# Optimization experiments

Hardware: AMD Instinct MI355X
Metric: run time of the kernel (lower is better)

Reference implementation:

```python
import jax, jax.numpy as jnp
import numpy as np

S, P, C = 64, 2048, 32   # num_scenes, num_pixels, scene_channels
A, D, E = 2048, 128, 64  # agent_size, dynamics_features, embed_dim


def setup_inputs() -> dict:
    key = jax.random.key(0)
    ks = jax.random.split(key, 9)
    inv = lambda n: 1.0 / np.sqrt(n)
    return {
        "global_scene": jax.random.normal(ks[0], (S, P, C), jnp.float32),
        "scene_idx": jax.random.randint(ks[1], (A,), 0, S),
        "dynamic_encoding": jax.random.normal(ks[2], (A, D), jnp.float32),
        "W_sn": jax.random.uniform(ks[3], (C, E), jnp.float32, -inv(C), inv(C)),
        "b_sn": jax.random.uniform(ks[4], (E,), jnp.float32, -inv(C), inv(C)),
        "W_df": jax.random.uniform(ks[5], (D, E), jnp.float32, -inv(D), inv(D)),
        "b_df": jax.random.uniform(ks[6], (E,), jnp.float32, -inv(D), inv(D)),
        "w_fc": jax.random.uniform(ks[7], (E,), jnp.float32, -inv(E), inv(E)),
        "b_fc": jax.random.uniform(ks[8], (1,), jnp.float32, -inv(E), inv(E)),
    }


def reference(global_scene, scene_idx, dynamic_encoding, W_sn, b_sn, W_df, b_df, w_fc, b_fc):
    # att1: [S, P, E]; att2: [A, E]
    att1 = jnp.einsum('spc,ce->spe', global_scene, W_sn) + b_sn
    att2 = dynamic_encoding @ W_df + b_df
    # gather scenes per agent, fuse add + relu: [A, P, E]
    add_fusion = jax.nn.relu(att1[scene_idx] + att2[:, None, :])
    # linear to scalar score per pixel, softmax over pixels (dim=1)
    logits = jnp.einsum('ape,e->ap', add_fusion, w_fc) + b_fc[0]  # [A, P]
    alpha = jax.nn.softmax(logits, axis=1)[:, :, None]            # [A, P, 1]
    # alpha-weighted pooling of gathered scene features -> [A, C]
    return jnp.sum(alpha * global_scene[scene_idx], axis=1)
```

## Files before the change

### kernel.cpp

```cpp
#include <hip/hip_runtime.h>
#include <hip/hip_bf16.h>

#define S_ 64
#define P_ 2048
#define C_ 32
#define A_ 2048
#define D_ 128
#define E_ 64

#define LPX   64
#define NLCH  (P_ / LPX)

__global__ __launch_bounds__(256) void att2s_kernel(
    const float* __restrict__ de, const float* __restrict__ Wdf,
    const float* __restrict__ bdf, const int* __restrict__ sidx,
    float* __restrict__ att2, int* __restrict__ counts,
    int* __restrict__ lists) {
  __shared__ float4 Wl[128 * 16];
  __shared__ float4 bl[16];
  __shared__ float  dl[16 * 128];
  const int tid = threadIdx.x;

  if (tid < 16) {
    const int a = blockIdx.x * 16 + tid;
    const int s = sidx[a];
    const int pos = atomicAdd(&counts[s], 1);
    lists[s * A_ + pos] = a;
  }

  const float4* W4 = (const float4*)Wdf;
#pragma unroll
  for (int i = 0; i < 8; ++i) Wl[tid + i * 256] = W4[tid + i * 256];
  if (tid < 16) bl[tid] = ((const float4*)bdf)[tid];
  const long base = (long)blockIdx.x * (16 * 128);
#pragma unroll
  for (int i = 0; i < 8; ++i) dl[tid + i * 256] = de[base + tid + i * 256];
  __syncthreads();

  const int r = tid >> 4, e4 = tid & 15;
  float4 acc = bl[e4];
#pragma unroll 4
  for (int d = 0; d < 128; ++d) {
    const float  g = dl[r * 128 + d];
    const float4 w = Wl[d * 16 + e4];
    acc.x = fmaf(g, w.x, acc.x);
    acc.y = fmaf(g, w.y, acc.y);
    acc.z = fmaf(g, w.z, acc.z);
    acc.w = fmaf(g, w.w, acc.w);
  }
  ((float4*)att2)[((long)blockIdx.x * 16 + r) * 16 + e4] = acc;
}

__global__ __launch_bounds__(256) void fused_kernel(
    const float* __restrict__ gs, const float* __restrict__ Wsn,
    const float* __restrict__ bsn, const float* __restrict__ wfc,
    const float* __restrict__ att2, const int* __restrict__ counts,
    const int* __restrict__ lists, float* __restrict__ out,
    float* __restrict__ Z) {
  const int s   = blockIdx.x >> 5;
  const int p0  = (blockIdx.x & (NLCH - 1)) * LPX;
  const int tid = threadIdx.x;
  const int px  = tid >> 2;
  const int eq  = tid & 3;

  __shared__ float  gsl[LPX][36];
  __shared__ float4 Wl4[32 * 16];
  __shared__ float4 a2l[32][16];
  __shared__ float  alpha_l[32][64];
  __shared__ int    aidl[32];

  const float4* W4 = (const float4*)Wsn;
  Wl4[tid]       = W4[tid];
  Wl4[tid + 256] = W4[tid + 256];

  const float4* g4 = (const float4*)(gs + ((long)s * P_ + p0) * C_);
#pragma unroll
  for (int k = 0; k < 2; ++k) {
    const int f = tid + k * 256;
    const float4 v = g4[f];
    const int pp = f >> 3, c0 = (f & 7) * 4;
    gsl[pp][c0]     = v.x;
    gsl[pp][c0 + 1] = v.y;
    gsl[pp][c0 + 2] = v.z;
    gsl[pp][c0 + 3] = v.w;
  }

  const float4* wf4 = (const float4*)wfc;
  const float4* b4  = (const float4*)bsn;
  float4 wf[4], a1[4];
#pragma unroll
  for (int q = 0; q < 4; ++q) { wf[q] = wf4[eq * 4 + q]; a1[q] = b4[eq * 4 + q]; }
  __syncthreads();

#pragma unroll
  for (int c = 0; c < 32; ++c) {
    const float g = gsl[px][c];
#pragma unroll
    for (int q = 0; q < 4; ++q) {
      const float4 w = Wl4[c * 16 + eq * 4 + q];
      a1[q].x = fmaf(g, w.x, a1[q].x);
      a1[q].y = fmaf(g, w.y, a1[q].y);
      a1[q].z = fmaf(g, w.z, a1[q].z);
      a1[q].w = fmaf(g, w.w, a1[q].w);
    }
  }

  const int j2 = tid >> 3;
  const int c4 = tid & 7;
  const int n_s = counts[s];

  for (int g0 = 0; g0 < n_s; g0 += 32) {
    const int m = min(32, n_s - g0);
    __syncthreads();
    if (tid < m) aidl[tid] = lists[s * A_ + g0 + tid];
    __syncthreads();
#pragma unroll
    for (int k = 0; k < 2; ++k) {
      const int idx = tid + k * 256;
      const int j = idx >> 4, e4 = idx & 15;
      if (j < m) a2l[j][e4] = ((const float4*)att2)[aidl[j] * 16 + e4];
    }
    __syncthreads();

    for (int j = 0; j < m; ++j) {
      const float4 t0 = a2l[j][eq * 4 + 0];
      const float4 t1 = a2l[j][eq * 4 + 1];
      const float4 t2 = a2l[j][eq * 4 + 2];
      const float4 t3 = a2l[j][eq * 4 + 3];
      float c0 = 0.f, c1 = 0.f, c2 = 0.f, c3 = 0.f;
      c0 = fmaf(fmaxf(a1[0].x + t0.x, 0.f), wf[0].x, c0);
      c1 = fmaf(fmaxf(a1[0].y + t0.y, 0.f), wf[0].y, c1);
      c2 = fmaf(fmaxf(a1[0].z + t0.z, 0.f), wf[0].z, c2);
      c3 = fmaf(fmaxf(a1[0].w + t0.w, 0.f), wf[0].w, c3);
      c0 = fmaf(fmaxf(a1[1].x + t1.x, 0.f), wf[1].x, c0);
      c1 = fmaf(fmaxf(a1[1].y + t1.y, 0.f), wf[1].y, c1);
      c2 = fmaf(fmaxf(a1[1].z + t1.z, 0.f), wf[1].z, c2);
      c3 = fmaf(fmaxf(a1[1].w + t1.w, 0.f), wf[1].w, c3);
      c0 = fmaf(fmaxf(a1[2].x + t2.x, 0.f), wf[2].x, c0);
      c1 = fmaf(fmaxf(a1[2].y + t2.y, 0.f), wf[2].y, c1);
      c2 = fmaf(fmaxf(a1[2].z + t2.z, 0.f), wf[2].z, c2);
      c3 = fmaf(fmaxf(a1[2].w + t2.w, 0.f), wf[2].w, c3);
      c0 = fmaf(fmaxf(a1[3].x + t3.x, 0.f), wf[3].x, c0);
      c1 = fmaf(fmaxf(a1[3].y + t3.y, 0.f), wf[3].y, c1);
      c2 = fmaf(fmaxf(a1[3].z + t3.z, 0.f), wf[3].z, c2);
      c3 = fmaf(fmaxf(a1[3].w + t3.w, 0.f), wf[3].w, c3);
      float r = (c0 + c1) + (c2 + c3);
      r += __shfl_xor(r, 1);
      r += __shfl_xor(r, 2);
      if (eq == 0) alpha_l[j][px] = __expf(r);
    }
    __syncthreads();

    if (j2 < m) {
      const int a = aidl[j2];
      float4 a0 = make_float4(0.f, 0.f, 0.f, 0.f);
      float4 a1p = make_float4(0.f, 0.f, 0.f, 0.f);
      float4 a2p = make_float4(0.f, 0.f, 0.f, 0.f);
      float4 a3p = make_float4(0.f, 0.f, 0.f, 0.f);
      float  zs = 0.f;
#pragma unroll 4
      for (int p4 = 0; p4 < LPX / 4; ++p4) {
        const float w0 = alpha_l[j2][p4 * 4 + 0];
        const float w1 = alpha_l[j2][p4 * 4 + 1];
        const float w2 = alpha_l[j2][p4 * 4 + 2];
        const float w3 = alpha_l[j2][p4 * 4 + 3];
        const float4 v0 = *(const float4*)&gsl[p4 * 4 + 0][c4 * 4];
        const float4 v1 = *(const float4*)&gsl[p4 * 4 + 1][c4 * 4];
        const float4 v2 = *(const float4*)&gsl[p4 * 4 + 2][c4 * 4];
        const float4 v3 = *(const float4*)&gsl[p4 * 4 + 3][c4 * 4];
        zs += (w0 + w1) + (w2 + w3);
        a0.x = fmaf(w0, v0.x, a0.x); a0.y = fmaf(w0, v0.y, a0.y);
        a0.z = fmaf(w0, v0.z, a0.z); a0.w = fmaf(w0, v0.w, a0.w);
        a1p.x = fmaf(w1, v1.x, a1p.x); a1p.y = fmaf(w1, v1.y, a1p.y);
        a1p.z = fmaf(w1, v1.z, a1p.z); a1p.w = fmaf(w1, v1.w, a1p.w);
        a2p.x = fmaf(w2, v2.x, a2p.x); a2p.y = fmaf(w2, v2.y, a2p.y);
        a2p.z = fmaf(w2, v2.z, a2p.z); a2p.w = fmaf(w2, v2.w, a2p.w);
        a3p.x = fmaf(w3, v3.x, a3p.x); a3p.y = fmaf(w3, v3.y, a3p.y);
        a3p.z = fmaf(w3, v3.z, a3p.z); a3p.w = fmaf(w3, v3.w, a3p.w);
      }
      const float4 acc = make_float4((a0.x + a1p.x) + (a2p.x + a3p.x),
                                     (a0.y + a1p.y) + (a2p.y + a3p.y),
                                     (a0.z + a1p.z) + (a2p.z + a3p.z),
                                     (a0.w + a1p.w) + (a2p.w + a3p.w));
      float* op = out + (long)a * C_ + c4 * 4;
      atomicAdd(op,     acc.x);
      atomicAdd(op + 1, acc.y);
      atomicAdd(op + 2, acc.z);
      atomicAdd(op + 3, acc.w);
      if (c4 == 0) atomicAdd(&Z[a], zs);
    }
  }
}

__global__ __launch_bounds__(256) void norm_kernel(
    float* __restrict__ out, const float* __restrict__ Z) {
  const int i = blockIdx.x * 256 + threadIdx.x;
  out[i] = out[i] / Z[i >> 5];
}

extern "C" void kernel_launch(void* const* d_in, const int* in_sizes, int n_in,
                              void* d_out, int out_size, void* d_ws, size_t ws_size,
                              hipStream_t stream) {
  const float* gs   = (const float*)d_in[0];
  const int*   sidx = (const int*)  d_in[1];
  const float* de   = (const float*)d_in[2];
  const float* Wsn  = (const float*)d_in[3];
  const float* bsn  = (const float*)d_in[4];
  const float* Wdf  = (const float*)d_in[5];
  const float* bdf  = (const float*)d_in[6];
  const float* wfc  = (const float*)d_in[7];
  float* out = (float*)d_out;

  float* att2   = (float*)d_ws;
  float* Z      = att2 + (long)A_ * E_;
  int*   counts = (int*)(Z + A_);
  int*   lists  = counts + 64;

  hipMemsetAsync(Z, 0, (A_ + 64) * sizeof(float), stream);
  hipMemsetAsync(out, 0, (size_t)out_size * sizeof(float), stream);

  att2s_kernel<<<A_ / 16,   256, 0, stream>>>(de, Wdf, bdf, sidx, att2,
                                              counts, lists);
  fused_kernel<<<S_ * NLCH, 256, 0, stream>>>(gs, Wsn, bsn, wfc, att2,
                                              counts, lists, out, Z);
  norm_kernel <<<(A_ * C_) / 256, 256, 0, stream>>>(out, Z);
}
```

Before: 161.9 us.

## Double pixel tile, use two threads per pixel, and fold zeroing into att2 kernel

The pixel chunk per block grows from 64 to 128, and each pixel is now handled by two threads with 32 embedding lanes each instead of four threads with 16. This halves the number of partial-sum atomics into out and Z, drops one cross-lane shuffle per agent, and amortises the per-block loads of W and the att2 rows over more pixels. The memsets of out and Z are replaced by zeroing inside att2s_kernel, leaving only a small memset for counts. In exchange there are half as many blocks and more registers per thread.

After: 151.1 us. -6.7%, faster.

```diff
diff --git a/kernel.cpp b/kernel.cpp
--- a/kernel.cpp
+++ b/kernel.cpp
@@ -8,18 +8,26 @@
 #define D_ 128
 #define E_ 64
 
-#define LPX   64
+#define LPX   128
 #define NLCH  (P_ / LPX)
 
 __global__ __launch_bounds__(256) void att2s_kernel(
     const float* __restrict__ de, const float* __restrict__ Wdf,
     const float* __restrict__ bdf, const int* __restrict__ sidx,
     float* __restrict__ att2, int* __restrict__ counts,
-    int* __restrict__ lists) {
+    int* __restrict__ lists, float* __restrict__ out, float* __restrict__ Z) {
   __shared__ float4 Wl[128 * 16];
   __shared__ float4 bl[16];
   __shared__ float  dl[16 * 128];
   const int tid = threadIdx.x;
+
+  {
+    const float4 z4 = make_float4(0.f, 0.f, 0.f, 0.f);
+    const int gidx = blockIdx.x * 256 + tid;
+    if (gidx < (A_ * C_) / 4)      ((float4*)out)[gidx] = z4;
+    else if (gidx < (A_ * C_) / 4 + A_ / 4)
+      ((float4*)Z)[gidx - (A_ * C_) / 4] = z4;
+  }
 
   if (tid < 16) {
     const int a = blockIdx.x * 16 + tid;
@@ -57,16 +65,16 @@
     const float* __restrict__ att2, const int* __restrict__ counts,
     const int* __restrict__ lists, float* __restrict__ out,
     float* __restrict__ Z) {
-  const int s   = blockIdx.x >> 5;
+  const int s   = blockIdx.x >> 4;
   const int p0  = (blockIdx.x & (NLCH - 1)) * LPX;
   const int tid = threadIdx.x;
-  const int px  = tid >> 2;
-  const int eq  = tid & 3;
+  const int px  = tid >> 1;
+  const int eh  = tid & 1;
 
   __shared__ float  gsl[LPX][36];
   __shared__ float4 Wl4[32 * 16];
   __shared__ float4 a2l[32][16];
-  __shared__ float  alpha_l[32][64];
+  __shared__ float  alpha_l[32][132];
   __shared__ int    aidl[32];
 
   const float4* W4 = (const float4*)Wsn;
@@ -75,7 +83,7 @@
 
   const float4* g4 = (const float4*)(gs + ((long)s * P_ + p0) * C_);
 #pragma unroll
-  for (int k = 0; k < 2; ++k) {
+  for (int k = 0; k < 4; ++k) {
     const int f = tid + k * 256;
     const float4 v = g4[f];
     const int pp = f >> 3, c0 = (f & 7) * 4;
@@ -87,17 +95,17 @@
 
   const float4* wf4 = (const float4*)wfc;
   const float4* b4  = (const float4*)bsn;
-  float4 wf[4], a1[4];
-#pragma unroll
-  for (int q = 0; q < 4; ++q) { wf[q] = wf4[eq * 4 + q]; a1[q] = b4[eq * 4 + q]; }
+  float4 wf[8], a1[8];
+#pragma unroll
+  for (int q = 0; q < 8; ++q) { wf[q] = wf4[eh * 8 + q]; a1[q] = b4[eh * 8 + q]; }
   __syncthreads();
 
 #pragma unroll
   for (int c = 0; c < 32; ++c) {
     const float g = gsl[px][c];
 #pragma unroll
-    for (int q = 0; q < 4; ++q) {
-      const float4 w = Wl4[c * 16 + eq * 4 + q];
+    for (int q = 0; q < 8; ++q) {
+      const float4 w = Wl4[c * 16 + eh * 8 + q];
       a1[q].x = fmaf(g, w.x, a1[q].x);
       a1[q].y = fmaf(g, w.y, a1[q].y);
       a1[q].z = fmaf(g, w.z, a1[q].z);
@@ -123,31 +131,20 @@
     __syncthreads();
 
     for (int j = 0; j < m; ++j) {
-      const float4 t0 = a2l[j][eq * 4 + 0];
-      const float4 t1 = a2l[j][eq * 4 + 1];
-      const float4 t2 = a2l[j][eq * 4 + 2];
-      const float4 t3 = a2l[j][eq * 4 + 3];
       float c0 = 0.f, c1 = 0.f, c2 = 0.f, c3 = 0.f;
-      c0 = fmaf(fmaxf(a1[0].x + t0.x, 0.f), wf[0].x, c0);
-      c1 = fmaf(fmaxf(a1[0].y + t0.y, 0.f), wf[0].y, c1);
-      c2 = fmaf(fmaxf(a1[0].z + t0.z, 0.f), wf[0].z, c2);
-      c3 = fmaf(fmaxf(a1[0].w + t0.w, 0.f), wf[0].w, c3);
-      c0 = fmaf(fmaxf(a1[1].x + t1.x, 0.f), wf[1].x, c0);
-      c1 = fmaf(fmaxf(a1[1].y + t1.y, 0.f), wf[1].y, c1);
-      c2 = fmaf(fmaxf(a1[1].z + t1.z, 0.f), wf[1].z, c2);
-      c3 = fmaf(fmaxf(a1[1].w + t1.w, 0.f), wf[1].w, c3);
-      c0 = fmaf(fmaxf(a1[2].x + t2.x, 0.f), wf[2].x, c0);
-      c1 = fmaf(fmaxf(a1[2].y + t2.y, 0.f), wf[2].y, c1);
-      c2 = fmaf(fmaxf(a1[2].z + t2.z, 0.f), wf[2].z, c2);
-      c3 = fmaf(fmaxf(a1[2].w + t2.w, 0.f), wf[2].w, c3);
-      c0 = fmaf(fmaxf(a1[3].x + t3.x, 0.f), wf[3].x, c0);
-      c1 = fmaf(fmaxf(a1[3].y + t3.y, 0.f), wf[3].y, c1);
-      c2 = fmaf(fmaxf(a1[3].z + t3.z, 0.f), wf[3].z, c2);
-      c3 = fmaf(fmaxf(a1[3].w + t3.w, 0.f), wf[3].w, c3);
+#pragma unroll
+      for (int q = 0; q < 8; ++q) {
+        const float4 t = a2l[j][eh * 8 + q];
+        const float4 w = wf[q];
+        const float4 av = a1[q];
+        c0 = fmaf(fmaxf(av.x + t.x, 0.f), w.x, c0);
+        c1 = fmaf(fmaxf(av.y + t.y, 0.f), w.y, c1);
+        c2 = fmaf(fmaxf(av.z + t.z, 0.f), w.z, c2);
+        c3 = fmaf(fmaxf(av.w + t.w, 0.f), w.w, c3);
+      }
       float r = (c0 + c1) + (c2 + c3);
       r += __shfl_xor(r, 1);
-      r += __shfl_xor(r, 2);
-      if (eq == 0) alpha_l[j][px] = __expf(r);
+      if (eh == 0) alpha_l[j][px] = __expf(r);
     }
     __syncthreads();
 
@@ -216,11 +213,9 @@
   int*   counts = (int*)(Z + A_);
   int*   lists  = counts + 64;
 
-  hipMemsetAsync(Z, 0, (A_ + 64) * sizeof(float), stream);
-  hipMemsetAsync(out, 0, (size_t)out_size * sizeof(float), stream);
-
+  hipMemsetAsync(counts, 0, 64 * sizeof(int), stream);
   att2s_kernel<<<A_ / 16,   256, 0, stream>>>(de, Wdf, bdf, sidx, att2,
-                                              counts, lists);
+                                              counts, lists, out, Z);
   fused_kernel<<<S_ * NLCH, 256, 0, stream>>>(gs, Wsn, bsn, wfc, att2,
                                               counts, lists, out, Z);
   norm_kernel <<<(A_ * C_) / 256, 256, 0, stream>>>(out, Z);
```
